# Kernel tuning notes

Hardware: AMD Instinct MI355X
Metric: run time of the kernel (lower is better)

## Reference

```python
import jax, jax.numpy as jnp
import numpy as np

N_NODES = 40000
N_EDGES = 640000
D_IN = 128
D_OUT = 128


def setup_inputs() -> dict:
    key = jax.random.key(0)
    k1, k2, k3 = jax.random.split(key, 3)
    x = jax.random.normal(k1, (N_NODES, D_IN), dtype=jnp.float32)
    W = jax.random.normal(k2, (D_IN, D_OUT), dtype=jnp.float32) / np.sqrt(D_IN)
    b = jnp.zeros((D_OUT,), dtype=jnp.float32)
    edge_index = jax.random.randint(k3, (2, N_EDGES), 0, N_NODES, dtype=jnp.int64)
    return {"x": x, "W": W, "b": b, "edge_index": edge_index}


def reference(x, W, b, edge_index):
    src, dst = edge_index[0], edge_index[1]
    n = x.shape[0]
    # asymmetric normalization: 1 / out-degree(src), inf -> 0
    deg = jax.ops.segment_sum(jnp.ones_like(src, dtype=x.dtype), src, num_segments=n)
    deg_inv = jnp.where(deg > 0, 1.0 / deg, 0.0)
    # GCNConv (add_self_loops=False, normalize=False): h = x @ W; msg_e = w_e * h[src_e]
    h = x @ W  # [N, D_OUT]
    msg = h[src] * deg_inv[src][:, None]  # [E, D_OUT] gather-weighted messages
    out = jax.ops.segment_sum(msg, dst, num_segments=n) + b  # scatter-add to dst
    return out
```

## Files before the change

### kernel.cpp

```cpp
#include <hip/hip_runtime.h>

#define N_NODES 40000
#define D 128
#define N_EDGES 640000
#define CAP 64
#define NSLICE 32
#define SLICE_E 20000
#define SLICE_E4 5000
#define HALF_BINS 20000
#define HALF_W 10000
#define WROW 20000
#define SRCHIST_BLKS 64
#define BIN_BLKS 625
#define GEMM_BLKS 1250
#define TOTAL_BLKS (SRCHIST_BLKS + BIN_BLKS + GEMM_BLKS)

static __device__ __forceinline__ unsigned short f2bf(float f) {
  unsigned u = __float_as_uint(f);
  return (unsigned short)((u + 0x7fffu + ((u >> 16) & 1u)) >> 16);
}
static __device__ __forceinline__ float bf2f(unsigned short h) {
  return __uint_as_float(((unsigned)h) << 16);
}

__global__ __launch_bounds__(256) void k_fused(
    const float* __restrict__ x, const float* __restrict__ W,
    const int* __restrict__ src, const int* __restrict__ dst,
    int* __restrict__ cnt_dst, unsigned* __restrict__ slabS,
    unsigned short* __restrict__ bucket, unsigned short* __restrict__ hb) {
  __shared__ unsigned smem[10240];
  const int bid = blockIdx.x;
  const int tid = threadIdx.x;

  if (bid < SRCHIST_BLKS) {
    const int b = bid >> 1;
    const int h = bid & 1;
    for (int i = tid; i < HALF_W; i += 256) smem[i] = 0;
    __syncthreads();
    const int4* p4 = (const int4*)(src + b * SLICE_E);
    const unsigned lo = (unsigned)(h * HALF_BINS);
    for (int it = tid; it < SLICE_E4; it += 256) {
      const int4 v = p4[it];
      unsigned u;
      u = (unsigned)v.x - lo; if (u < HALF_BINS) atomicAdd(&smem[u >> 1], 1u << ((u & 1) * 16));
      u = (unsigned)v.y - lo; if (u < HALF_BINS) atomicAdd(&smem[u >> 1], 1u << ((u & 1) * 16));
      u = (unsigned)v.z - lo; if (u < HALF_BINS) atomicAdd(&smem[u >> 1], 1u << ((u & 1) * 16));
      u = (unsigned)v.w - lo; if (u < HALF_BINS) atomicAdd(&smem[u >> 1], 1u << ((u & 1) * 16));
    }
    __syncthreads();
    unsigned* row = slabS + (size_t)b * WROW + h * HALF_W;
    for (int i = tid; i < HALF_W; i += 256) row[i] = smem[i];
    return;
  }

  const int t = bid - SRCHIST_BLKS;
  const int r3 = t % 3;

  if (r3 == 2) {
    const int cid = t / 3;
    const int e0 = (cid * 256 + tid) * 4;
    const int4 s4 = *(const int4*)(src + e0);
    const int4 d4 = *(const int4*)(dst + e0);
    int r;
    r = atomicAdd(&cnt_dst[d4.x], 1);
    if (r < CAP) bucket[(size_t)d4.x * CAP + r] = (unsigned short)s4.x;
    r = atomicAdd(&cnt_dst[d4.y], 1);
    if (r < CAP) bucket[(size_t)d4.y * CAP + r] = (unsigned short)s4.y;
    r = atomicAdd(&cnt_dst[d4.z], 1);
    if (r < CAP) bucket[(size_t)d4.z * CAP + r] = (unsigned short)s4.z;
    r = atomicAdd(&cnt_dst[d4.w], 1);
    if (r < CAP) bucket[(size_t)d4.w * CAP + r] = (unsigned short)s4.w;
    return;
  }

  const int gid = 2 * (t / 3) + r3;
  float* wl = (float*)smem;
  float* xl = wl + 4096;
  const int n0 = gid * 32;
  const int td = tid & 31;
  const int tn = tid >> 5;

  {
    const float4* xg = (const float4*)(x + (size_t)n0 * D);
    float4* xl4 = (float4*)xl;
#pragma unroll
    for (int j = 0; j < 4; ++j) xl4[tid + j * 256] = xg[tid + j * 256];
  }

  float acc[4][4];
#pragma unroll
  for (int a = 0; a < 4; ++a)
#pragma unroll
    for (int q = 0; q < 4; ++q) acc[a][q] = 0.0f;

  for (int c = 0; c < 4; ++c) {
    __syncthreads();
    {
      const float4* wg = (const float4*)(W + (size_t)c * 32 * D);
      float4* wl4 = (float4*)wl;
#pragma unroll
      for (int j = 0; j < 4; ++j) wl4[tid + j * 256] = wg[tid + j * 256];
    }
    __syncthreads();
#pragma unroll 8
    for (int k = 0; k < 32; ++k) {
      const int kk = c * 32 + k;
      float4 wv = ((const float4*)wl)[k * 32 + td];
#pragma unroll
      for (int a = 0; a < 4; ++a) {
        float xa = xl[(tn * 4 + a) * D + kk];
        acc[a][0] += xa * wv.x;
        acc[a][1] += xa * wv.y;
        acc[a][2] += xa * wv.z;
        acc[a][3] += xa * wv.w;
      }
    }
  }

#pragma unroll
  for (int a = 0; a < 4; ++a) {
    const int n = n0 + tn * 4 + a;
    ushort4 v;
    v.x = f2bf(acc[a][0]);
    v.y = f2bf(acc[a][1]);
    v.z = f2bf(acc[a][2]);
    v.w = f2bf(acc[a][3]);
    ((ushort4*)(hb + (size_t)n * D))[td] = v;
  }
}

__global__ __launch_bounds__(256) void k_colsum_src(
    const unsigned* __restrict__ slabS, int* __restrict__ cnt_src) {
  const int w = blockIdx.x * 256 + threadIdx.x;
  if (w >= WROW) return;
  unsigned run = 0;
#pragma unroll 8
  for (int b = 0; b < NSLICE; ++b) run += slabS[(size_t)b * WROW + w];
  cnt_src[2 * w] = (int)(run & 0xFFFFu);
  cnt_src[2 * w + 1] = (int)(run >> 16);
}

__global__ __launch_bounds__(256) void k_gather(
    const int* __restrict__ cnt_dst, const int* __restrict__ cnt_src,
    const unsigned short* __restrict__ bucket,
    const unsigned short* __restrict__ hb,
    const float* __restrict__ b, float* __restrict__ out) {
  const int tid = threadIdx.x;
  const int node = blockIdx.x * 8 + (tid >> 5);
  const int lane = tid & 31;

  int len = cnt_dst[node];
  if (len > CAP) len = CAP;
  const unsigned short* bk = bucket + (size_t)node * CAP;

  float4 a0 = {0.f, 0.f, 0.f, 0.f};
  float4 a1 = {0.f, 0.f, 0.f, 0.f};
  float4 a2 = {0.f, 0.f, 0.f, 0.f};
  float4 a3 = {0.f, 0.f, 0.f, 0.f};

  int j = 0;
  for (; j + 3 < len; j += 4) {
    const int s0 = bk[j + 0];
    const int s1 = bk[j + 1];
    const int s2 = bk[j + 2];
    const int s3 = bk[j + 3];
    const float f0 = 1.0f / (float)cnt_src[s0];
    const float f1 = 1.0f / (float)cnt_src[s1];
    const float f2 = 1.0f / (float)cnt_src[s2];
    const float f3 = 1.0f / (float)cnt_src[s3];
    ushort4 u0 = ((const ushort4*)(hb + (size_t)s0 * D))[lane];
    ushort4 u1 = ((const ushort4*)(hb + (size_t)s1 * D))[lane];
    ushort4 u2 = ((const ushort4*)(hb + (size_t)s2 * D))[lane];
    ushort4 u3 = ((const ushort4*)(hb + (size_t)s3 * D))[lane];
    a0.x += f0 * bf2f(u0.x); a0.y += f0 * bf2f(u0.y); a0.z += f0 * bf2f(u0.z); a0.w += f0 * bf2f(u0.w);
    a1.x += f1 * bf2f(u1.x); a1.y += f1 * bf2f(u1.y); a1.z += f1 * bf2f(u1.z); a1.w += f1 * bf2f(u1.w);
    a2.x += f2 * bf2f(u2.x); a2.y += f2 * bf2f(u2.y); a2.z += f2 * bf2f(u2.z); a2.w += f2 * bf2f(u2.w);
    a3.x += f3 * bf2f(u3.x); a3.y += f3 * bf2f(u3.y); a3.z += f3 * bf2f(u3.z); a3.w += f3 * bf2f(u3.w);
  }
  for (; j < len; ++j) {
    const int s0 = bk[j];
    const float f0 = 1.0f / (float)cnt_src[s0];
    ushort4 u0 = ((const ushort4*)(hb + (size_t)s0 * D))[lane];
    a0.x += f0 * bf2f(u0.x); a0.y += f0 * bf2f(u0.y); a0.z += f0 * bf2f(u0.z); a0.w += f0 * bf2f(u0.w);
  }

  const float4 bias = ((const float4*)b)[lane];
  float4 v;
  v.x = bias.x + (a0.x + a1.x) + (a2.x + a3.x);
  v.y = bias.y + (a0.y + a1.y) + (a2.y + a3.y);
  v.z = bias.z + (a0.z + a1.z) + (a2.z + a3.z);
  v.w = bias.w + (a0.w + a1.w) + (a2.w + a3.w);
  ((float4*)(out + (size_t)node * D))[lane] = v;
}

extern "C" void kernel_launch(void* const* d_in, const int* in_sizes, int n_in,
                              void* d_out, int out_size, void* d_ws, size_t ws_size,
                              hipStream_t stream) {
  const float* x = (const float*)d_in[0];
  const float* W = (const float*)d_in[1];
  const float* b = (const float*)d_in[2];
  const int* ei = (const int*)d_in[3];
  const int* src = ei;
  const int* dst = ei + N_EDGES;
  float* out = (float*)d_out;

  char* ws = (char*)d_ws;
  int* cnt_dst = (int*)(ws + 0);
  int* cnt_src = (int*)(ws + 160000);
  unsigned* slabS = (unsigned*)(ws + 320000);
  unsigned short* bucket = (unsigned short*)(ws + 2880000);
  unsigned short* hb = (unsigned short*)(ws + 8000000);

  hipMemsetAsync(cnt_dst, 0, 160000, stream);
  k_fused<<<TOTAL_BLKS, 256, 0, stream>>>(x, W, src, dst, cnt_dst, slabS,
                                          bucket, hb);
  k_colsum_src<<<79, 256, 0, stream>>>(slabS, cnt_src);
  k_gather<<<5000, 256, 0, stream>>>(cnt_dst, cnt_src, bucket, hb, b, out);
}
```

Measured before the change: 77.22 us.

## Use bf16 MFMA for x@W with prepacked W and precomputed inverse degrees

Replaces the FP32 FMA GEMM tile with bf16 MFMA 16x16x32 instructions on 64-row tiles. W is pre-packed into an MFMA fragment layout by a new prep kernel, which also zeroes cnt_dst in place of the memset. The column-sum kernel now writes reciprocal degrees so the gather loads a float instead of dividing per edge. This lowers the precision of x before the matmul, and the hb stores become scattered 2-byte writes.

```diff
diff --git a/kernel.cpp b/kernel.cpp
--- a/kernel.cpp
+++ b/kernel.cpp
@@ -12,8 +12,11 @@
 #define WROW 20000
 #define SRCHIST_BLKS 64
 #define BIN_BLKS 625
-#define GEMM_BLKS 1250
-#define TOTAL_BLKS (SRCHIST_BLKS + BIN_BLKS + GEMM_BLKS)
+#define GEMM_BLKS 625
+#define XPAD 132
+
+typedef __attribute__((ext_vector_type(8))) short short8_t;
+typedef __attribute__((ext_vector_type(4))) float float4_t;
 
 static __device__ __forceinline__ unsigned short f2bf(float f) {
   unsigned u = __float_as_uint(f);
@@ -23,8 +26,28 @@
   return __uint_as_float(((unsigned)h) << 16);
 }
 
+__global__ __launch_bounds__(256) void k_prep(const float* __restrict__ W,
+                                              unsigned short* __restrict__ Wb,
+                                              int* __restrict__ cnt_dst) {
+  const int bid = blockIdx.x;
+  const int tid = threadIdx.x;
+  if (bid < 64) {
+    const int g = bid * 256 + tid;
+    const int j = g & 7;
+    const int lane = (g >> 3) & 63;
+    const int q = (g >> 9) & 3;
+    const int t = g >> 11;
+    const int k = q * 32 + (lane >> 4) * 8 + j;
+    const int d = t * 16 + (lane & 15);
+    Wb[g] = f2bf(W[k * D + d]);
+  } else {
+    const int i = (bid - 64) * 256 + tid;
+    if (i < N_NODES) cnt_dst[i] = 0;
+  }
+}
+
 __global__ __launch_bounds__(256) void k_fused(
-    const float* __restrict__ x, const float* __restrict__ W,
+    const float* __restrict__ x, const unsigned short* __restrict__ Wb,
     const int* __restrict__ src, const int* __restrict__ dst,
     int* __restrict__ cnt_dst, unsigned* __restrict__ slabS,
     unsigned short* __restrict__ bucket, unsigned short* __restrict__ hb) {
@@ -54,10 +77,9 @@
   }
 
   const int t = bid - SRCHIST_BLKS;
-  const int r3 = t % 3;
-
-  if (r3 == 2) {
-    const int cid = t / 3;
+
+  if (t & 1) {
+    const int cid = t >> 1;
     const int e0 = (cid * 256 + tid) * 4;
     const int4 s4 = *(const int4*)(src + e0);
     const int4 d4 = *(const int4*)(dst + e0);
@@ -73,75 +95,74 @@
     return;
   }
 
-  const int gid = 2 * (t / 3) + r3;
-  float* wl = (float*)smem;
-  float* xl = wl + 4096;
-  const int n0 = gid * 32;
-  const int td = tid & 31;
-  const int tn = tid >> 5;
-
+  const int gid = t >> 1;
+  const int n0 = gid * 64;
+  const int w = tid >> 6;
+  const int lane = tid & 63;
+
+  float* xl = (float*)smem;
   {
     const float4* xg = (const float4*)(x + (size_t)n0 * D);
-    float4* xl4 = (float4*)xl;
-#pragma unroll
-    for (int j = 0; j < 4; ++j) xl4[tid + j * 256] = xg[tid + j * 256];
-  }
-
-  float acc[4][4];
-#pragma unroll
-  for (int a = 0; a < 4; ++a)
-#pragma unroll
-    for (int q = 0; q < 4; ++q) acc[a][q] = 0.0f;
-
-  for (int c = 0; c < 4; ++c) {
-    __syncthreads();
-    {
-      const float4* wg = (const float4*)(W + (size_t)c * 32 * D);
-      float4* wl4 = (float4*)wl;
-#pragma unroll
-      for (int j = 0; j < 4; ++j) wl4[tid + j * 256] = wg[tid + j * 256];
-    }
-    __syncthreads();
-#pragma unroll 8
-    for (int k = 0; k < 32; ++k) {
-      const int kk = c * 32 + k;
-      float4 wv = ((const float4*)wl)[k * 32 + td];
-#pragma unroll
-      for (int a = 0; a < 4; ++a) {
-        float xa = xl[(tn * 4 + a) * D + kk];
-        acc[a][0] += xa * wv.x;
-        acc[a][1] += xa * wv.y;
-        acc[a][2] += xa * wv.z;
-        acc[a][3] += xa * wv.w;
-      }
-    }
-  }
-
-#pragma unroll
-  for (int a = 0; a < 4; ++a) {
-    const int n = n0 + tn * 4 + a;
-    ushort4 v;
-    v.x = f2bf(acc[a][0]);
-    v.y = f2bf(acc[a][1]);
-    v.z = f2bf(acc[a][2]);
-    v.w = f2bf(acc[a][3]);
-    ((ushort4*)(hb + (size_t)n * D))[td] = v;
+#pragma unroll
+    for (int j = 0; j < 8; ++j) {
+      const int idx = tid + j * 256;
+      const int row = idx >> 5;
+      const int c4 = idx & 31;
+      ((float4*)(xl + row * XPAD))[c4] = xg[idx];
+    }
+  }
+  __syncthreads();
+
+  short8_t afrag[4];
+  {
+    const float* ap0 = xl + (w * 16 + (lane & 15)) * XPAD + (lane >> 4) * 8;
+#pragma unroll
+    for (int q = 0; q < 4; ++q) {
+      const float* ap = ap0 + q * 32;
+      const float4 v0 = *(const float4*)ap;
+      const float4 v1 = *(const float4*)(ap + 4);
+      short8_t a;
+      a[0] = (short)f2bf(v0.x); a[1] = (short)f2bf(v0.y);
+      a[2] = (short)f2bf(v0.z); a[3] = (short)f2bf(v0.w);
+      a[4] = (short)f2bf(v1.x); a[5] = (short)f2bf(v1.y);
+      a[6] = (short)f2bf(v1.z); a[7] = (short)f2bf(v1.w);
+      afrag[q] = a;
+    }
+  }
+
+  const int orow = n0 + w * 16 + (lane >> 4) * 4;
+  const int ocolbase = lane & 15;
+#pragma unroll
+  for (int t8 = 0; t8 < 8; ++t8) {
+    float4_t acc = {0.f, 0.f, 0.f, 0.f};
+#pragma unroll
+    for (int q = 0; q < 4; ++q) {
+      const short8_t bfrag =
+          *(const short8_t*)(Wb + ((size_t)(t8 * 4 + q) * 64 + lane) * 8);
+      acc = __builtin_amdgcn_mfma_f32_16x16x32_bf16(afrag[q], bfrag, acc, 0, 0, 0);
+    }
+    const int col = t8 * 16 + ocolbase;
+#pragma unroll
+    for (int r = 0; r < 4; ++r)
+      hb[(size_t)(orow + r) * D + col] = f2bf(acc[r]);
   }
 }
 
 __global__ __launch_bounds__(256) void k_colsum_src(
-    const unsigned* __restrict__ slabS, int* __restrict__ cnt_src) {
+    const unsigned* __restrict__ slabS, float* __restrict__ dinv) {
   const int w = blockIdx.x * 256 + threadIdx.x;
   if (w >= WROW) return;
   unsigned run = 0;
 #pragma unroll 8
   for (int b = 0; b < NSLICE; ++b) run += slabS[(size_t)b * WROW + w];
-  cnt_src[2 * w] = (int)(run & 0xFFFFu);
-  cnt_src[2 * w + 1] = (int)(run >> 16);
+  const unsigned lo = run & 0xFFFFu;
+  const unsigned hi = run >> 16;
+  dinv[2 * w] = lo ? 1.0f / (float)lo : 0.0f;
+  dinv[2 * w + 1] = hi ? 1.0f / (float)hi : 0.0f;
 }
 
 __global__ __launch_bounds__(256) void k_gather(
-    const int* __restrict__ cnt_dst, const int* __restrict__ cnt_src,
+    const int* __restrict__ cnt_dst, const float* __restrict__ dinv,
     const unsigned short* __restrict__ bucket,
     const unsigned short* __restrict__ hb,
     const float* __restrict__ b, float* __restrict__ out) {
@@ -164,10 +185,10 @@
     const int s1 = bk[j + 1];
     const int s2 = bk[j + 2];
     const int s3 = bk[j + 3];
-    const float f0 = 1.0f / (float)cnt_src[s0];
-    const float f1 = 1.0f / (float)cnt_src[s1];
-    const float f2 = 1.0f / (float)cnt_src[s2];
-    const float f3 = 1.0f / (float)cnt_src[s3];
+    const float f0 = dinv[s0];
+    const float f1 = dinv[s1];
+    const float f2 = dinv[s2];
+    const float f3 = dinv[s3];
     ushort4 u0 = ((const ushort4*)(hb + (size_t)s0 * D))[lane];
     ushort4 u1 = ((const ushort4*)(hb + (size_t)s1 * D))[lane];
     ushort4 u2 = ((const ushort4*)(hb + (size_t)s2 * D))[lane];
@@ -179,7 +200,7 @@
   }
   for (; j < len; ++j) {
     const int s0 = bk[j];
-    const float f0 = 1.0f / (float)cnt_src[s0];
+    const float f0 = dinv[s0];
     ushort4 u0 = ((const ushort4*)(hb + (size_t)s0 * D))[lane];
     a0.x += f0 * bf2f(u0.x); a0.y += f0 * bf2f(u0.y); a0.z += f0 * bf2f(u0.z); a0.w += f0 * bf2f(u0.w);
   }
@@ -206,14 +227,15 @@
 
   char* ws = (char*)d_ws;
   int* cnt_dst = (int*)(ws + 0);
-  int* cnt_src = (int*)(ws + 160000);
+  float* dinv = (float*)(ws + 160000);
   unsigned* slabS = (unsigned*)(ws + 320000);
-  unsigned short* bucket = (unsigned short*)(ws + 2880000);
-  unsigned short* hb = (unsigned short*)(ws + 8000000);
-
-  hipMemsetAsync(cnt_dst, 0, 160000, stream);
-  k_fused<<<TOTAL_BLKS, 256, 0, stream>>>(x, W, src, dst, cnt_dst, slabS,
-                                          bucket, hb);
-  k_colsum_src<<<79, 256, 0, stream>>>(slabS, cnt_src);
-  k_gather<<<5000, 256, 0, stream>>>(cnt_dst, cnt_src, bucket, hb, b, out);
-}
+  unsigned short* Wb = (unsigned short*)(ws + 2880000);
+  unsigned short* bucket = (unsigned short*)(ws + 2912768);
+  unsigned short* hb = (unsigned short*)(ws + 8032768);
+
+  k_prep<<<221, 256, 0, stream>>>(W, Wb, cnt_dst);
+  k_fused<<<SRCHIST_BLKS + BIN_BLKS + GEMM_BLKS, 256, 0, stream>>>(
+      x, Wb, src, dst, cnt_dst, slabS, bucket, hb);
+  k_colsum_src<<<79, 256, 0, stream>>>(slabS, dinv);
+  k_gather<<<5000, 256, 0, stream>>>(cnt_dst, dinv, bucket, hb, b, out);
+}
```

Result: no change. 76.76 us (-0.6%).
